# Kernel optimization log

Hardware: AMD Instinct MI355X
Metric: run time of the kernel (lower is better)

## Reference

```python
import jax, jax.numpy as jnp
import numpy as np


def setup_inputs() -> dict:
    key = jax.random.key(0)
    ks = jax.random.split(key, 6)
    shapes = [
        (2048, 128, 64),   # large: shape[1] > 64
        (2048, 32, 32),    # small -> fused bucket
        (2048, 64, 64),    # small (== 64 is not > 64) -> fused bucket
        (2048, 16, 48),    # small -> fused bucket
        (2048, 200, 32),   # large: shape[1] > 64
        (2048, 8, 8),      # small -> fused bucket
    ]
    inp = {f"x{i}": jax.random.normal(ks[i], s, dtype=jnp.float32) for i, s in enumerate(shapes)}
    inp["dim"] = 1  # dim[0] in the original module: reduce over the middle (list-length) axis
    return inp


def reference(x0, x1, x2, x3, x4, x5, dim):
    # ComboSumModule: outputs[i] = input_list[i].sum(dim[0]).
    # The size-bucketing (shape[1]>64 or shape[2]>64) only changes kernel
    # fusion, not the math, so each tensor is reduced independently.
    xs = (x0, x1, x2, x3, x4, x5)
    return tuple(jnp.sum(x, axis=dim) for x in xs)
```

## Files before the change

kernel.cpp:

```cpp
#include <hip/hip_runtime.h>


__device__ __forceinline__ float4 f4add(float4 a, float4 b) {
  return make_float4(a.x + b.x, a.y + b.y, a.z + b.z, a.w + b.w);
}

template <int M, int N>
__device__ __forceinline__ void col_sum(const float* __restrict__ xp,
                                        float* __restrict__ out,
                                        int local, int wave, int lane,
                                        int out_base4, float4* lds) {
  constexpr int N4 = N / 4;
  constexpr int R = M / 4;
  static_assert(R % 2 == 0, "R divisible by 2");
  const int b  = local / N4;
  const int n4 = local - b * N4;
  const float4* __restrict__ p =
      reinterpret_cast<const float4*>(xp) + (size_t)b * (M * N4) +
      (size_t)(wave * R) * N4 + n4;

  float4 a0 = make_float4(0.f, 0.f, 0.f, 0.f);
  float4 a1 = make_float4(0.f, 0.f, 0.f, 0.f);
#pragma unroll 2
  for (int m = 0; m < R; m += 2) {
    float4 v0 = p[(size_t)(m + 0) * N4];
    float4 v1 = p[(size_t)(m + 1) * N4];
    a0 = f4add(a0, v0);
    a1 = f4add(a1, v1);
  }
  lds[wave * 64 + lane] = f4add(a0, a1);
  __syncthreads();
  if (wave == 0) {
    float4 r = f4add(f4add(lds[lane], lds[64 + lane]),
                     f4add(lds[128 + lane], lds[192 + lane]));
    reinterpret_cast<float4*>(out)[out_base4 + local] = r;
  }
}

__global__ __launch_bounds__(256) void ComboSumModule_25314537242674_kernel(
    const float* __restrict__ x0, const float* __restrict__ x1,
    const float* __restrict__ x2, const float* __restrict__ x3,
    const float* __restrict__ x4, const float* __restrict__ x5,
    float* __restrict__ out) {
  __shared__ float4 lds[4 * 64];
  const int lane = threadIdx.x & 63;
  const int wave = threadIdx.x >> 6;
  const int u = blockIdx.x * 64 + lane;
  if (u < 32768) {
    col_sum<128, 64>(x0, out, u, wave, lane, 0, lds);
  } else if (u < 49152) {
    col_sum<32, 32>(x1, out, u - 32768, wave, lane, 32768, lds);
  } else if (u < 81920) {
    col_sum<64, 64>(x2, out, u - 49152, wave, lane, 49152, lds);
  } else if (u < 106496) {
    col_sum<16, 48>(x3, out, u - 81920, wave, lane, 81920, lds);
  } else if (u < 122880) {
    col_sum<200, 32>(x4, out, u - 106496, wave, lane, 106496, lds);
  } else {
    col_sum<8, 8>(x5, out, u - 122880, wave, lane, 122880, lds);
  }
}

extern "C" void kernel_launch(void* const* d_in, const int* in_sizes, int n_in,
                              void* d_out, int out_size, void* d_ws, size_t ws_size,
                              hipStream_t stream) {
  const float* x0 = (const float*)d_in[0];
  const float* x1 = (const float*)d_in[1];
  const float* x2 = (const float*)d_in[2];
  const float* x3 = (const float*)d_in[3];
  const float* x4 = (const float*)d_in[4];
  const float* x5 = (const float*)d_in[5];
  float* out = (float*)d_out;

  ComboSumModule_25314537242674_kernel<<<1984, 256, 0, stream>>>(
      x0, x1, x2, x3, x4, x5, out);
}
```

Before: 182.6 us.

## Rebalance per-tensor work with 1024-thread blocks and variable wave splits

Each block now has 16 waves instead of 4. How the rows are split across waves depends on the tensor: large reductions use all 16 waves, small ones group several output tiles per block, and the 8x8 tensor skips the LDS reduction. The goal is more even load balance (x4's 200 rows split into 12/13-row chunks) and more parallelism per column tile, with four independent accumulators to keep more loads in flight. The cost is larger blocks with a 16 KB LDS buffer and a full-block barrier, which may reduce scheduling flexibility.

```diff
diff --git a/kernel.cpp b/kernel.cpp
--- a/kernel.cpp
+++ b/kernel.cpp
@@ -5,59 +5,83 @@
   return make_float4(a.x + b.x, a.y + b.y, a.z + b.z, a.w + b.w);
 }
 
-template <int M, int N>
-__device__ __forceinline__ void col_sum(const float* __restrict__ xp,
-                                        float* __restrict__ out,
-                                        int local, int wave, int lane,
-                                        int out_base4, float4* lds) {
+template <int M, int N, int WPG>
+__device__ __forceinline__ void region(const float* __restrict__ xp,
+                                       float* __restrict__ out,
+                                       int out_base4, int group, int wave,
+                                       int lane, int row_start, int row_cnt,
+                                       float4* lds) {
   constexpr int N4 = N / 4;
-  constexpr int R = M / 4;
-  static_assert(R % 2 == 0, "R divisible by 2");
-  const int b  = local / N4;
-  const int n4 = local - b * N4;
+  const int u = group * 64 + lane;
+  const int b = u / N4;
+  const int n4 = u - b * N4;
   const float4* __restrict__ p =
       reinterpret_cast<const float4*>(xp) + (size_t)b * (M * N4) +
-      (size_t)(wave * R) * N4 + n4;
+      (size_t)row_start * N4 + n4;
 
   float4 a0 = make_float4(0.f, 0.f, 0.f, 0.f);
   float4 a1 = make_float4(0.f, 0.f, 0.f, 0.f);
-#pragma unroll 2
-  for (int m = 0; m < R; m += 2) {
-    float4 v0 = p[(size_t)(m + 0) * N4];
-    float4 v1 = p[(size_t)(m + 1) * N4];
+  float4 a2 = make_float4(0.f, 0.f, 0.f, 0.f);
+  float4 a3 = make_float4(0.f, 0.f, 0.f, 0.f);
+  int i = 0;
+#pragma unroll
+  for (; i + 4 <= row_cnt; i += 4) {
+    float4 v0 = p[(size_t)(i + 0) * N4];
+    float4 v1 = p[(size_t)(i + 1) * N4];
+    float4 v2 = p[(size_t)(i + 2) * N4];
+    float4 v3 = p[(size_t)(i + 3) * N4];
     a0 = f4add(a0, v0);
     a1 = f4add(a1, v1);
+    a2 = f4add(a2, v2);
+    a3 = f4add(a3, v3);
   }
-  lds[wave * 64 + lane] = f4add(a0, a1);
+  for (; i < row_cnt; ++i)
+    a0 = f4add(a0, p[(size_t)i * N4]);
+
+  float4 r = f4add(f4add(a0, a1), f4add(a2, a3));
+
+  if (WPG == 1) {
+    reinterpret_cast<float4*>(out)[out_base4 + group * 64 + lane] = r;
+    return;
+  }
+  lds[wave * 64 + lane] = r;
   __syncthreads();
-  if (wave == 0) {
-    float4 r = f4add(f4add(lds[lane], lds[64 + lane]),
-                     f4add(lds[128 + lane], lds[192 + lane]));
-    reinterpret_cast<float4*>(out)[out_base4 + local] = r;
+  if ((wave & (WPG - 1)) == 0) {
+    float4 s = lds[wave * 64 + lane];
+#pragma unroll
+    for (int j = 1; j < WPG; ++j) s = f4add(s, lds[(wave + j) * 64 + lane]);
+    reinterpret_cast<float4*>(out)[out_base4 + group * 64 + lane] = s;
   }
 }
 
-__global__ __launch_bounds__(256) void ComboSumModule_25314537242674_kernel(
+__global__ __launch_bounds__(1024) void ComboSumModule_25314537242674_kernel(
     const float* __restrict__ x0, const float* __restrict__ x1,
     const float* __restrict__ x2, const float* __restrict__ x3,
     const float* __restrict__ x4, const float* __restrict__ x5,
     float* __restrict__ out) {
-  __shared__ float4 lds[4 * 64];
+  __shared__ float4 lds[16 * 64];
   const int lane = threadIdx.x & 63;
   const int wave = threadIdx.x >> 6;
-  const int u = blockIdx.x * 64 + lane;
-  if (u < 32768) {
-    col_sum<128, 64>(x0, out, u, wave, lane, 0, lds);
-  } else if (u < 49152) {
-    col_sum<32, 32>(x1, out, u - 32768, wave, lane, 32768, lds);
-  } else if (u < 81920) {
-    col_sum<64, 64>(x2, out, u - 49152, wave, lane, 49152, lds);
-  } else if (u < 106496) {
-    col_sum<16, 48>(x3, out, u - 81920, wave, lane, 81920, lds);
-  } else if (u < 122880) {
-    col_sum<200, 32>(x4, out, u - 106496, wave, lane, 106496, lds);
+  const int blk = blockIdx.x;
+
+  if (blk < 256) {
+    const int cnt = (wave < 8) ? 13 : 12;
+    const int start = 12 * wave + ((wave < 8) ? wave : 8);
+    region<200, 32, 16>(x4, out, 106496, blk, wave, lane, start, cnt, lds);
+  } else if (blk < 768) {
+    region<128, 64, 16>(x0, out, 0, blk - 256, wave, lane, 8 * wave, 8, lds);
+  } else if (blk < 1024) {
+    const int g = (blk - 768) * 2 + (wave >> 3);
+    region<64, 64, 8>(x2, out, 49152, g, wave, lane, 8 * (wave & 7), 8, lds);
+  } else if (blk < 1088) {
+    const int g = (blk - 1024) * 4 + (wave >> 2);
+    region<32, 32, 4>(x1, out, 32768, g, wave, lane, 8 * (wave & 3), 8, lds);
+  } else if (blk < 1136) {
+    const int g = (blk - 1088) * 8 + (wave >> 1);
+    region<16, 48, 2>(x3, out, 81920, g, wave, lane, 8 * (wave & 1), 8, lds);
   } else {
-    col_sum<8, 8>(x5, out, u - 122880, wave, lane, 122880, lds);
+    const int g = (blk - 1136) * 16 + wave;
+    region<8, 8, 1>(x5, out, 122880, g, wave, lane, 0, 8, lds);
   }
 }
 
@@ -72,6 +96,6 @@
   const float* x5 = (const float*)d_in[5];
   float* out = (float*)d_out;
 
-  ComboSumModule_25314537242674_kernel<<<1984, 256, 0, stream>>>(
+  ComboSumModule_25314537242674_kernel<<<1140, 1024, 0, stream>>>(
       x0, x1, x2, x3, x4, x5, out);
 }
```

Measured after the change: 178.0 us. 2.5% less time.

## Remap column-sum work to per-wave batch streaming with shuffle reductions

Applied to the files above, without the earlier changes.

Replaces the block-level column sum, where four waves split the reduced axis and combine through LDS with a barrier, with per-wave mappings. Each wave now streams one or more whole batches with contiguous coalesced float4 loads and reduces across lanes with xor shuffles, using special paths for the 16x48 and 8x8 tensors. This removes the LDS traffic and __syncthreads and the idle waves in the final combine, and cuts the grid from 1984 to 1444 blocks. In exchange it adds shuffle instructions, and per-wave load imbalance between tensor segments may limit the gain.

```diff
diff --git a/kernel.cpp b/kernel.cpp
--- a/kernel.cpp
+++ b/kernel.cpp
@@ -5,35 +5,37 @@
   return make_float4(a.x + b.x, a.y + b.y, a.z + b.z, a.w + b.w);
 }
 
-template <int M, int N>
-__device__ __forceinline__ void col_sum(const float* __restrict__ xp,
-                                        float* __restrict__ out,
-                                        int local, int wave, int lane,
-                                        int out_base4, float4* lds) {
-  constexpr int N4 = N / 4;
-  constexpr int R = M / 4;
-  static_assert(R % 2 == 0, "R divisible by 2");
-  const int b  = local / N4;
-  const int n4 = local - b * N4;
-  const float4* __restrict__ p =
-      reinterpret_cast<const float4*>(xp) + (size_t)b * (M * N4) +
-      (size_t)(wave * R) * N4 + n4;
+__device__ __forceinline__ float4 f4shfl_xor(float4 v, int mask) {
+  return make_float4(__shfl_xor(v.x, mask), __shfl_xor(v.y, mask),
+                     __shfl_xor(v.z, mask), __shfl_xor(v.w, mask));
+}
 
-  float4 a0 = make_float4(0.f, 0.f, 0.f, 0.f);
-  float4 a1 = make_float4(0.f, 0.f, 0.f, 0.f);
-#pragma unroll 2
-  for (int m = 0; m < R; m += 2) {
-    float4 v0 = p[(size_t)(m + 0) * N4];
-    float4 v1 = p[(size_t)(m + 1) * N4];
-    a0 = f4add(a0, v0);
-    a1 = f4add(a1, v1);
-  }
-  lds[wave * 64 + lane] = f4add(a0, a1);
-  __syncthreads();
-  if (wave == 0) {
-    float4 r = f4add(f4add(lds[lane], lds[64 + lane]),
-                     f4add(lds[128 + lane], lds[192 + lane]));
-    reinterpret_cast<float4*>(out)[out_base4 + local] = r;
+template <int M, int N4, int CHUNKS>
+__device__ __forceinline__ void stream_sum(const float* __restrict__ xp,
+                                           float* __restrict__ out,
+                                           int out_base4, int first_batch,
+                                           int lane) {
+  constexpr int LOADS = (M * N4) / 64;
+  static_assert((M * N4) % 64 == 0 && 64 % N4 == 0, "layout");
+  const int col = lane & (N4 - 1);
+#pragma unroll
+  for (int c = 0; c < CHUNKS; ++c) {
+    const int b = first_batch + c;
+    const float4* __restrict__ p =
+        reinterpret_cast<const float4*>(xp) + (size_t)b * (M * N4) + lane;
+    float4 a0 = make_float4(0.f, 0.f, 0.f, 0.f);
+    float4 a1 = make_float4(0.f, 0.f, 0.f, 0.f);
+#pragma unroll
+    for (int i = 0; i + 2 <= LOADS; i += 2) {
+      a0 = f4add(a0, p[(size_t)i * 64]);
+      a1 = f4add(a1, p[(size_t)(i + 1) * 64]);
+    }
+    if (LOADS & 1) a0 = f4add(a0, p[(size_t)(LOADS - 1) * 64]);
+    float4 r = f4add(a0, a1);
+#pragma unroll
+    for (int mask = N4; mask < 64; mask <<= 1) r = f4add(r, f4shfl_xor(r, mask));
+    if (lane < N4)
+      reinterpret_cast<float4*>(out)[out_base4 + b * N4 + col] = r;
   }
 }
 
@@ -42,22 +44,48 @@
     const float* __restrict__ x2, const float* __restrict__ x3,
     const float* __restrict__ x4, const float* __restrict__ x5,
     float* __restrict__ out) {
-  __shared__ float4 lds[4 * 64];
   const int lane = threadIdx.x & 63;
-  const int wave = threadIdx.x >> 6;
-  const int u = blockIdx.x * 64 + lane;
-  if (u < 32768) {
-    col_sum<128, 64>(x0, out, u, wave, lane, 0, lds);
-  } else if (u < 49152) {
-    col_sum<32, 32>(x1, out, u - 32768, wave, lane, 32768, lds);
-  } else if (u < 81920) {
-    col_sum<64, 64>(x2, out, u - 49152, wave, lane, 49152, lds);
-  } else if (u < 106496) {
-    col_sum<16, 48>(x3, out, u - 81920, wave, lane, 81920, lds);
-  } else if (u < 122880) {
-    col_sum<200, 32>(x4, out, u - 106496, wave, lane, 106496, lds);
+  const int gw = blockIdx.x * 4 + (threadIdx.x >> 6);
+
+  if (gw < 2048) {
+    stream_sum<128, 16, 1>(x0, out, 0, gw, lane);
+  } else if (gw < 4096) {
+    stream_sum<200, 8, 1>(x4, out, 106496, gw - 2048, lane);
+  } else if (gw < 5120) {
+    stream_sum<64, 16, 2>(x2, out, 49152, (gw - 4096) * 2, lane);
+  } else if (gw < 5376) {
+    stream_sum<32, 8, 8>(x1, out, 32768, (gw - 5120) * 8, lane);
+  } else if (gw < 5760) {
+    const int u = (gw - 5376) * 64 + lane;
+    const int b = u / 12;
+    const int n4 = u - b * 12;
+    const float4* __restrict__ p =
+        reinterpret_cast<const float4*>(x3) + (size_t)b * 192 + n4;
+    float4 a0 = make_float4(0.f, 0.f, 0.f, 0.f);
+    float4 a1 = make_float4(0.f, 0.f, 0.f, 0.f);
+#pragma unroll
+    for (int i = 0; i < 16; i += 2) {
+      a0 = f4add(a0, p[(size_t)i * 12]);
+      a1 = f4add(a1, p[(size_t)(i + 1) * 12]);
+    }
+    reinterpret_cast<float4*>(out)[81920 + u] = f4add(a0, a1);
   } else {
-    col_sum<8, 8>(x5, out, u - 122880, wave, lane, 122880, lds);
+    const int wi = gw - 5760;
+    const int f = lane & 15;
+    const int bs = lane >> 4;
+    const float4* __restrict__ p =
+        reinterpret_cast<const float4*>(x5) + (size_t)wi * 128 * 16 + lane;
+#pragma unroll 4
+    for (int j = 0; j < 32; ++j) {
+      float4 r = p[(size_t)j * 64];
+      r = f4add(r, f4shfl_xor(r, 2));
+      r = f4add(r, f4shfl_xor(r, 4));
+      r = f4add(r, f4shfl_xor(r, 8));
+      if (f < 2) {
+        const int b = wi * 128 + j * 4 + bs;
+        reinterpret_cast<float4*>(out)[122880 + b * 2 + f] = r;
+      }
+    }
   }
 }
 
@@ -72,6 +100,6 @@
   const float* x5 = (const float*)d_in[5];
   float* out = (float*)d_out;
 
-  ComboSumModule_25314537242674_kernel<<<1984, 256, 0, stream>>>(
+  ComboSumModule_25314537242674_kernel<<<1444, 256, 0, stream>>>(
       x0, x1, x2, x3, x4, x5, out);
 }
```

After: 193.0 us. +5.7%, slower.
